# Optimization experiments

Hardware: AMD Instinct MI355X
Metric: run time of the kernel (lower is better)

The kernel has to match this reference:

```python
import jax, jax.numpy as jnp
import numpy as np

NUM_USERS = 100000
NUM_ITEMS = 50000
N = NUM_USERS + NUM_ITEMS
D = 64
NNZ = 4000000
BATCH = 8192
NUM_LAYERS = 3


def setup_inputs() -> dict:
    key = jax.random.key(0)
    k = jax.random.split(key, 8)
    return {
        "user_emb": jax.random.normal(k[0], (NUM_USERS, D), jnp.float32) * 0.1,
        "item_emb": jax.random.normal(k[1], (NUM_ITEMS, D), jnp.float32) * 0.1,
        # symmetric-normalized adjacency values (positive, ~1/degree scale)
        "adj_vals": jax.random.uniform(k[2], (NNZ,), jnp.float32) * (1.0 / 13.0),
        "adj_rows": jax.random.randint(k[3], (NNZ,), 0, N, jnp.int32),
        "adj_cols": jax.random.randint(k[4], (NNZ,), 0, N, jnp.int32),
        "user_idx": jax.random.randint(k[5], (BATCH,), 0, NUM_USERS, jnp.int32),
        "pos_idx": jax.random.randint(k[6], (BATCH,), 0, NUM_ITEMS, jnp.int32),
        "neg_idx": jax.random.randint(k[7], (BATCH,), 0, NUM_ITEMS, jnp.int32),
    }


def _propagate(user_emb, item_emb, adj_vals, adj_rows, adj_cols):
    # E0 = concat(user table, item table) along node axis -> [N, D]
    e = jnp.concatenate([user_emb, item_emb], axis=0)
    acc = e  # running sum over layer embeddings (E0 included)
    for _ in range(NUM_LAYERS):
        # SpMM: E <- A_norm @ E, via gather on cols + segment_sum on rows
        msg = adj_vals[:, None] * e[adj_cols]  # [NNZ, D]
        e = jax.ops.segment_sum(msg, adj_rows, num_segments=N)
        acc = acc + e
    final = acc / jnp.asarray(NUM_LAYERS + 1, e.dtype)  # mean-pool over layers
    return final


def reference(user_emb, item_emb, adj_vals, adj_rows, adj_cols,
              user_idx, pos_idx, neg_idx):
    final = _propagate(user_emb, item_emb, adj_vals, adj_rows, adj_cols)
    # split into user/item tables, then gather BPR triplets
    u = final[user_idx]                     # [B, D]
    p = final[NUM_USERS + pos_idx]          # [B, D]
    n = final[NUM_USERS + neg_idx]          # [B, D]
    pos_score = jnp.sum(u * p, axis=-1, keepdims=True)  # Dot(axes=1) -> [B,1]
    neg_score = jnp.sum(u * n, axis=-1, keepdims=True)
    return pos_score - neg_score
```

## Files before the change

kernel.cpp:

```cpp
#include <hip/hip_runtime.h>
#include <hip/hip_bf16.h>

#define D 64
#define MAXNB 1024
#define BIN_T 512
#define BIN_CHUNK 8192
#define BIN_EPT (BIN_CHUNK / BIN_T)
#define BUCKET_BITS 8
#define BUCKET_SIZE 256
#define COL_MASK 0x3FFFF
#define ROW_SHIFT 18

static __device__ __forceinline__ float bf_lo(unsigned v) {
  return __uint_as_float(v << 16);
}
static __device__ __forceinline__ float bf_hi(unsigned v) {
  return __uint_as_float(v & 0xffff0000u);
}
static __device__ __forceinline__ unsigned pack_bf2(float a, float b) {
  __hip_bfloat16 x = __float2bfloat16(a);
  __hip_bfloat16 y = __float2bfloat16(b);
  unsigned short ux = *reinterpret_cast<unsigned short*>(&x);
  unsigned short uy = *reinterpret_cast<unsigned short*>(&y);
  return (unsigned)ux | ((unsigned)uy << 16);
}

__global__ __launch_bounds__(256) void convert_kernel(
    const float4* __restrict__ ue, const float4* __restrict__ ie,
    uint2* __restrict__ out, int nu4, int total4,
    int* __restrict__ counts, int nbp1,
    const int* __restrict__ ui, const int* __restrict__ pi,
    const int* __restrict__ ni, int* __restrict__ list, int batch, int nu) {
  int i = blockIdx.x * blockDim.x + threadIdx.x;
  if (i < nbp1) counts[i] = 0;
  if (i < batch) {
    list[3 * i] = ui[i];
    list[3 * i + 1] = nu + pi[i];
    list[3 * i + 2] = nu + ni[i];
  }
  if (i >= total4) return;
  float4 v = (i < nu4) ? ue[i] : ie[i - nu4];
  out[i] = make_uint2(pack_bf2(v.x, v.y), pack_bf2(v.z, v.w));
}

__global__ __launch_bounds__(256) void bucket_hist_kernel(
    const int* __restrict__ rows, int* __restrict__ counts, int nnz, int nb) {
  __shared__ int h[MAXNB];
  int t = threadIdx.x;
  for (int i = t; i < nb; i += 256) h[i] = 0;
  __syncthreads();
  for (int e = blockIdx.x * 256 + t; e < nnz; e += gridDim.x * 256)
    atomicAdd(&h[rows[e] >> BUCKET_BITS], 1);
  __syncthreads();
  for (int i = t; i < nb; i += 256)
    if (h[i]) atomicAdd(&counts[i], h[i]);
}

__global__ __launch_bounds__(1024) void bucket_scan_kernel(
    const int* __restrict__ counts, int* __restrict__ base,
    int* __restrict__ cursor, int nb) {
  __shared__ int lds[1024];
  int t = threadIdx.x;
  int v = (t < nb) ? counts[t] : 0;
  lds[t] = v;
  __syncthreads();
  for (int off = 1; off < 1024; off <<= 1) {
    int add = (t >= off) ? lds[t - off] : 0;
    __syncthreads();
    lds[t] += add;
    __syncthreads();
  }
  if (t < nb) {
    base[t + 1] = lds[t];
    cursor[t + 1] = lds[t];
  }
  if (t == 0) {
    base[0] = 0;
    cursor[0] = 0;
  }
}

__global__ __launch_bounds__(BIN_T) void bin_kernel(
    const float* __restrict__ vals, const int* __restrict__ rows,
    const int* __restrict__ cols, int* __restrict__ cursor,
    int2* __restrict__ binned, int nnz, int nb) {
  __shared__ int lh[MAXNB];
  int t = threadIdx.x;
  long long base_e = (long long)blockIdx.x * BIN_CHUNK;
  int end_e = (int)((base_e + BIN_CHUNK < (long long)nnz) ? base_e + BIN_CHUNK
                                                          : (long long)nnz);
  for (int i = t; i < nb; i += BIN_T) lh[i] = 0;
  __syncthreads();
  int r[BIN_EPT];
  #pragma unroll
  for (int k = 0; k < BIN_EPT; ++k) {
    int e = (int)base_e + k * BIN_T + t;
    if (e < end_e) {
      r[k] = rows[e];
      atomicAdd(&lh[r[k] >> BUCKET_BITS], 1);
    } else {
      r[k] = -1;
    }
  }
  __syncthreads();
  for (int i = t; i < nb; i += BIN_T) {
    int c = lh[i];
    if (c) lh[i] = atomicAdd(&cursor[i], c);
  }
  __syncthreads();
  #pragma unroll
  for (int k = 0; k < BIN_EPT; ++k) {
    int e = (int)base_e + k * BIN_T + t;
    if (e < end_e) {
      int pos = atomicAdd(&lh[r[k] >> BUCKET_BITS], 1);
      binned[pos] = make_int2((cols[e] & COL_MASK) |
                                  ((r[k] & (BUCKET_SIZE - 1)) << ROW_SHIFT),
                              __float_as_int(vals[e]));
    }
  }
}

__global__ __launch_bounds__(512) void place_kernel(
    const int2* __restrict__ binned, const int* __restrict__ base,
    int2* __restrict__ edges, int* __restrict__ row_start, int nrows, int nb) {
  __shared__ int rh[BUCKET_SIZE];
  __shared__ int cur[BUCKET_SIZE];
  int b = blockIdx.x;
  int t = threadIdx.x;
  int start = base[b];
  int end = base[b + 1];
  int r0 = b << BUCKET_BITS;
  if (t < BUCKET_SIZE) rh[t] = 0;
  __syncthreads();
  for (int i = start + t; i < end; i += 512)
    atomicAdd(&rh[((unsigned)binned[i].x) >> ROW_SHIFT], 1);
  __syncthreads();
  int myc = (t < BUCKET_SIZE) ? rh[t] : 0;
  for (int off = 1; off < BUCKET_SIZE; off <<= 1) {
    int add = (t >= off && t < BUCKET_SIZE) ? rh[t - off] : 0;
    __syncthreads();
    if (t < BUCKET_SIZE) rh[t] += add;
    __syncthreads();
  }
  if (t < BUCKET_SIZE) {
    int excl = rh[t] - myc;
    int r = r0 + t;
    if (r < nrows) row_start[r] = start + excl;
    if (b == nb - 1 && t == 0) row_start[nrows] = end;
    cur[t] = start + excl;
  }
  __syncthreads();
  for (int i = start + t; i < end; i += 512) {
    int2 rec = binned[i];
    unsigned x = (unsigned)rec.x;
    int pos = atomicAdd(&cur[x >> ROW_SHIFT], 1);
    edges[pos] = make_int2((int)(x & COL_MASK), rec.y);
  }
}

__global__ __launch_bounds__(256) void spmm_bf16_kernel(
    const int* __restrict__ row_start, const int2* __restrict__ edges,
    const uint4* __restrict__ src,
    uint4* __restrict__ dst, int nrows) {
  int wid = (int)(((long long)blockIdx.x * blockDim.x + threadIdx.x) >> 6);
  if (wid >= nrows) return;
  int lane = threadIdx.x & 63;
  int sub = lane >> 3;
  int d8 = lane & 7;
  int s = row_start[wid];
  int e = row_start[wid + 1];
  float a0 = 0.f, a1 = 0.f, a2 = 0.f, a3 = 0.f;
  float a4 = 0.f, a5 = 0.f, a6 = 0.f, a7 = 0.f;
  int j = s;
  for (; j + 16 <= e; j += 16) {
    int2 E[2];
    uint4 V[2];
    #pragma unroll
    for (int k = 0; k < 2; ++k) E[k] = edges[j + 8 * k + sub];
    #pragma unroll
    for (int k = 0; k < 2; ++k)
      V[k] = src[((unsigned)E[k].x << 3) + (unsigned)d8];
    #pragma unroll
    for (int k = 0; k < 2; ++k) {
      float w = __int_as_float(E[k].y);
      a0 = fmaf(w, bf_lo(V[k].x), a0);
      a1 = fmaf(w, bf_hi(V[k].x), a1);
      a2 = fmaf(w, bf_lo(V[k].y), a2);
      a3 = fmaf(w, bf_hi(V[k].y), a3);
      a4 = fmaf(w, bf_lo(V[k].z), a4);
      a5 = fmaf(w, bf_hi(V[k].z), a5);
      a6 = fmaf(w, bf_lo(V[k].w), a6);
      a7 = fmaf(w, bf_hi(V[k].w), a7);
    }
  }
  for (; j < e; j += 8) {
    int idx = j + sub;
    bool ok = idx < e;
    int2 ed = edges[ok ? idx : (e - 1)];
    uint4 v = src[((unsigned)ed.x << 3) + (unsigned)d8];
    float w = ok ? __int_as_float(ed.y) : 0.f;
    a0 = fmaf(w, bf_lo(v.x), a0);
    a1 = fmaf(w, bf_hi(v.x), a1);
    a2 = fmaf(w, bf_lo(v.y), a2);
    a3 = fmaf(w, bf_hi(v.y), a3);
    a4 = fmaf(w, bf_lo(v.z), a4);
    a5 = fmaf(w, bf_hi(v.z), a5);
    a6 = fmaf(w, bf_lo(v.w), a6);
    a7 = fmaf(w, bf_hi(v.w), a7);
  }
  #pragma unroll
  for (int off = 32; off >= 8; off >>= 1) {
    a0 += __shfl_down(a0, off, 64);
    a1 += __shfl_down(a1, off, 64);
    a2 += __shfl_down(a2, off, 64);
    a3 += __shfl_down(a3, off, 64);
    a4 += __shfl_down(a4, off, 64);
    a5 += __shfl_down(a5, off, 64);
    a6 += __shfl_down(a6, off, 64);
    a7 += __shfl_down(a7, off, 64);
  }
  if (lane < 8)
    dst[((unsigned)wid << 3) + (unsigned)d8] =
        make_uint4(pack_bf2(a0, a1), pack_bf2(a2, a3),
                   pack_bf2(a4, a5), pack_bf2(a6, a7));
}

__global__ __launch_bounds__(256) void spmm_bf16_list_kernel(
    const int* __restrict__ row_start, const int2* __restrict__ edges,
    const uint4* __restrict__ src, uint4* __restrict__ dst,
    const int* __restrict__ list, int nlist) {
  int widx = (int)(((long long)blockIdx.x * blockDim.x + threadIdx.x) >> 6);
  if (widx >= nlist) return;
  int wid = list[widx];
  int lane = threadIdx.x & 63;
  int sub = lane >> 3;
  int d8 = lane & 7;
  int s = row_start[wid];
  int e = row_start[wid + 1];
  float a0 = 0.f, a1 = 0.f, a2 = 0.f, a3 = 0.f;
  float a4 = 0.f, a5 = 0.f, a6 = 0.f, a7 = 0.f;
  int j = s;
  for (; j + 16 <= e; j += 16) {
    int2 E[2];
    uint4 V[2];
    #pragma unroll
    for (int k = 0; k < 2; ++k) E[k] = edges[j + 8 * k + sub];
    #pragma unroll
    for (int k = 0; k < 2; ++k)
      V[k] = src[((unsigned)E[k].x << 3) + (unsigned)d8];
    #pragma unroll
    for (int k = 0; k < 2; ++k) {
      float w = __int_as_float(E[k].y);
      a0 = fmaf(w, bf_lo(V[k].x), a0);
      a1 = fmaf(w, bf_hi(V[k].x), a1);
      a2 = fmaf(w, bf_lo(V[k].y), a2);
      a3 = fmaf(w, bf_hi(V[k].y), a3);
      a4 = fmaf(w, bf_lo(V[k].z), a4);
      a5 = fmaf(w, bf_hi(V[k].z), a5);
      a6 = fmaf(w, bf_lo(V[k].w), a6);
      a7 = fmaf(w, bf_hi(V[k].w), a7);
    }
  }
  for (; j < e; j += 8) {
    int idx = j + sub;
    bool ok = idx < e;
    int2 ed = edges[ok ? idx : (e - 1)];
    uint4 v = src[((unsigned)ed.x << 3) + (unsigned)d8];
    float w = ok ? __int_as_float(ed.y) : 0.f;
    a0 = fmaf(w, bf_lo(v.x), a0);
    a1 = fmaf(w, bf_hi(v.x), a1);
    a2 = fmaf(w, bf_lo(v.y), a2);
    a3 = fmaf(w, bf_hi(v.y), a3);
    a4 = fmaf(w, bf_lo(v.z), a4);
    a5 = fmaf(w, bf_hi(v.z), a5);
    a6 = fmaf(w, bf_lo(v.w), a6);
    a7 = fmaf(w, bf_hi(v.w), a7);
  }
  #pragma unroll
  for (int off = 32; off >= 8; off >>= 1) {
    a0 += __shfl_down(a0, off, 64);
    a1 += __shfl_down(a1, off, 64);
    a2 += __shfl_down(a2, off, 64);
    a3 += __shfl_down(a3, off, 64);
    a4 += __shfl_down(a4, off, 64);
    a5 += __shfl_down(a5, off, 64);
    a6 += __shfl_down(a6, off, 64);
    a7 += __shfl_down(a7, off, 64);
  }
  if (lane < 8)
    dst[((unsigned)wid << 3) + (unsigned)d8] =
        make_uint4(pack_bf2(a0, a1), pack_bf2(a2, a3),
                   pack_bf2(a4, a5), pack_bf2(a6, a7));
}

__global__ __launch_bounds__(256) void score2_kernel(
    const float* __restrict__ ue, const float* __restrict__ ie,
    const unsigned* __restrict__ e1, const unsigned* __restrict__ e2,
    const unsigned* __restrict__ e3, const int* __restrict__ ui,
    const int* __restrict__ pi, const int* __restrict__ ni,
    float* __restrict__ out, int batch, int nu) {
  int w = (int)(((long long)blockIdx.x * blockDim.x + threadIdx.x) >> 6);
  int lane = threadIdx.x & 63;
  int half = lane >> 5;
  int d2 = lane & 31;
  int b = w * 2 + half;
  if (b >= batch) return;
  long long un = (long long)ui[b];
  int p = pi[b], n = ni[b];
  long long pn = (long long)(nu + p);
  long long nn_ = (long long)(nu + n);
  float2 U = *(const float2*)(ue + (un << 6) + (d2 << 1));
  float2 P = *(const float2*)(ie + ((long long)p << 6) + (d2 << 1));
  float2 Nv = *(const float2*)(ie + ((long long)n << 6) + (d2 << 1));
  unsigned v;
  v = e1[(un << 5) + d2]; U.x += bf_lo(v); U.y += bf_hi(v);
  v = e2[(un << 5) + d2]; U.x += bf_lo(v); U.y += bf_hi(v);
  v = e3[(un << 5) + d2]; U.x += bf_lo(v); U.y += bf_hi(v);
  v = e1[(pn << 5) + d2]; P.x += bf_lo(v); P.y += bf_hi(v);
  v = e2[(pn << 5) + d2]; P.x += bf_lo(v); P.y += bf_hi(v);
  v = e3[(pn << 5) + d2]; P.x += bf_lo(v); P.y += bf_hi(v);
  v = e1[(nn_ << 5) + d2]; Nv.x += bf_lo(v); Nv.y += bf_hi(v);
  v = e2[(nn_ << 5) + d2]; Nv.x += bf_lo(v); Nv.y += bf_hi(v);
  v = e3[(nn_ << 5) + d2]; Nv.x += bf_lo(v); Nv.y += bf_hi(v);
  float s = U.x * (P.x - Nv.x) + U.y * (P.y - Nv.y);
  #pragma unroll
  for (int off = 16; off; off >>= 1) s += __shfl_down(s, off, 32);
  if (d2 == 0) out[b] = s * (1.0f / 16.0f);
}

__global__ __launch_bounds__(256) void init_kernel(
    const float4* __restrict__ ue, const float4* __restrict__ ie,
    float4* __restrict__ e, float4* __restrict__ acc, int nu4, int total4) {
  int i = blockIdx.x * blockDim.x + threadIdx.x;
  if (i >= total4) return;
  float4 v = (i < nu4) ? ue[i] : ie[i - nu4];
  e[i] = v;
  acc[i] = v;
}

__global__ __launch_bounds__(256) void scatter_kernel(
    const float* __restrict__ vals, const int* __restrict__ rows,
    const int* __restrict__ cols, const float* __restrict__ src,
    float* __restrict__ dst, int nnz) {
  long long gid = (long long)blockIdx.x * blockDim.x + threadIdx.x;
  int e = (int)(gid >> 6);
  if (e >= nnz) return;
  int d = (int)(gid & 63);
  float w = vals[e];
  float x = src[((long long)cols[e] << 6) + d];
  atomicAdd(dst + (((long long)rows[e] << 6) + d), w * x);
}

__global__ __launch_bounds__(256) void acc_kernel(
    float4* __restrict__ acc, const float4* __restrict__ e, int total4) {
  int i = blockIdx.x * blockDim.x + threadIdx.x;
  if (i >= total4) return;
  float4 a = acc[i];
  float4 b = e[i];
  a.x += b.x; a.y += b.y; a.z += b.z; a.w += b.w;
  acc[i] = a;
}

__global__ __launch_bounds__(256) void score_kernel(
    const float* __restrict__ acc, const int* __restrict__ ui,
    const int* __restrict__ pi, const int* __restrict__ ni,
    float* __restrict__ out, int batch, int nu) {
  int wid = (int)(((long long)blockIdx.x * blockDim.x + threadIdx.x) >> 6);
  int lane = threadIdx.x & 63;
  if (wid >= batch) return;
  int u = ui[wid];
  int p = pi[wid];
  int n = ni[wid];
  float uv = acc[((long long)u << 6) + lane];
  float pv = acc[((long long)(nu + p) << 6) + lane];
  float nv = acc[((long long)(nu + n) << 6) + lane];
  float s = uv * (pv - nv);
  #pragma unroll
  for (int off = 32; off; off >>= 1) s += __shfl_down(s, off, 64);
  if (lane == 0) out[wid] = s * (1.0f / 16.0f);
}

static inline size_t align_up(size_t x) { return (x + 255) & ~(size_t)255; }

extern "C" void kernel_launch(void* const* d_in, const int* in_sizes, int n_in,
                              void* d_out, int out_size, void* d_ws, size_t ws_size,
                              hipStream_t stream) {
  const float* user_emb = (const float*)d_in[0];
  const float* item_emb = (const float*)d_in[1];
  const float* adj_vals = (const float*)d_in[2];
  const int* adj_rows = (const int*)d_in[3];
  const int* adj_cols = (const int*)d_in[4];
  const int* user_idx = (const int*)d_in[5];
  const int* pos_idx = (const int*)d_in[6];
  const int* neg_idx = (const int*)d_in[7];

  const int nnz = in_sizes[2];
  const int batch = in_sizes[5];
  const int nu = in_sizes[0] / D;
  const int ni = in_sizes[1] / D;
  const int nrows = nu + ni;
  const int nb = (nrows + BUCKET_SIZE - 1) / BUCKET_SIZE;
  const long long nd = (long long)nrows * D;
  const size_t nd_bytes = (size_t)nd * sizeof(float);
  const size_t bf_tbl = align_up((size_t)nrows * D * 2);
  const size_t edges_bytes = align_up((size_t)nnz * 8);

  const int total4 = (int)(nd / 4);
  const int nu4 = nu * D / 4;
  const int ew_blocks = (total4 + 255) / 256;

  const size_t need = 4 * bf_tbl + 2 * edges_bytes +
                      align_up((size_t)(nrows + 1) * 4) +
                      3 * align_up((size_t)(nb + 1) * 4) +
                      align_up((size_t)(3 * batch) * 4);
  const bool fast = (ws_size >= need) && (nb <= MAXNB) && (nrows <= COL_MASK);

  if (fast) {
    char* wp = (char*)d_ws;
    unsigned* e0b = (unsigned*)wp;    wp += bf_tbl;
    unsigned* e1 = (unsigned*)wp;     wp += bf_tbl;
    unsigned* e2 = (unsigned*)wp;     wp += bf_tbl;
    unsigned* e3 = (unsigned*)wp;     wp += bf_tbl;
    int2* edges = (int2*)wp;          wp += edges_bytes;
    int2* binned = (int2*)wp;         wp += edges_bytes;
    int* row_start = (int*)wp;        wp += align_up((size_t)(nrows + 1) * 4);
    int* base = (int*)wp;             wp += align_up((size_t)(nb + 1) * 4);
    int* counts = (int*)wp;           wp += align_up((size_t)(nb + 1) * 4);
    int* cursor = (int*)wp;           wp += align_up((size_t)(nb + 1) * 4);
    int* list = (int*)wp;

    convert_kernel<<<ew_blocks, 256, 0, stream>>>(
        (const float4*)user_emb, (const float4*)item_emb,
        (uint2*)e0b, nu4, total4, counts, nb + 1,
        user_idx, pos_idx, neg_idx, list, batch, nu);

    bucket_hist_kernel<<<1024, 256, 0, stream>>>(adj_rows, counts, nnz, nb);
    bucket_scan_kernel<<<1, 1024, 0, stream>>>(counts, base, cursor, nb);

    bin_kernel<<<(nnz + BIN_CHUNK - 1) / BIN_CHUNK, BIN_T, 0, stream>>>(
        adj_vals, adj_rows, adj_cols, cursor, binned, nnz, nb);
    place_kernel<<<nb, 512, 0, stream>>>(binned, base, edges, row_start,
                                         nrows, nb);

    const int spmm_blocks = (nrows + 3) / 4;
    spmm_bf16_kernel<<<spmm_blocks, 256, 0, stream>>>(
        row_start, edges, (const uint4*)e0b, (uint4*)e1, nrows);
    spmm_bf16_kernel<<<spmm_blocks, 256, 0, stream>>>(
        row_start, edges, (const uint4*)e1, (uint4*)e2, nrows);
    const int nlist = 3 * batch;
    spmm_bf16_list_kernel<<<(nlist + 3) / 4, 256, 0, stream>>>(
        row_start, edges, (const uint4*)e2, (uint4*)e3, list, nlist);

    score2_kernel<<<(batch / 2 + 3) / 4, 256, 0, stream>>>(
        user_emb, item_emb, e1, e2, e3, user_idx, pos_idx, neg_idx,
        (float*)d_out, batch, nu);
  } else {
    char* wp = (char*)d_ws;
    float* acc = (float*)wp;          wp += nd_bytes;
    float* e_a = (float*)wp;          wp += nd_bytes;
    float* e_b = (float*)wp;

    init_kernel<<<ew_blocks, 256, 0, stream>>>(
        (const float4*)user_emb, (const float4*)item_emb,
        (float4*)e_a, (float4*)acc, nu4, total4);
    const long long scatter_work = (long long)nnz * 64;
    const int scatter_blocks = (int)((scatter_work + 255) / 256);
    float* src = e_a;
    float* dst = e_b;
    for (int layer = 0; layer < 3; ++layer) {
      hipMemsetAsync(dst, 0, nd_bytes, stream);
      scatter_kernel<<<scatter_blocks, 256, 0, stream>>>(adj_vals, adj_rows,
                                                         adj_cols, src, dst, nnz);
      acc_kernel<<<ew_blocks, 256, 0, stream>>>((float4*)acc, (const float4*)dst,
                                                total4);
      float* t = src; src = dst; dst = t;
    }
    score_kernel<<<(batch + 3) / 4, 256, 0, stream>>>(
        acc, user_idx, pos_idx, neg_idx, (float*)d_out, batch, nu);
  }
}
```

Measured before the change: 291.9 us.

## Stage binned edges in LDS for coalesced bucket writes; widen buckets

The bin kernel now sorts each chunk's edges by bucket inside shared memory, using a block-wide prefix scan over bucket counts. It then writes them to global memory contiguously, finding each element's bucket by binary search, instead of scattering each edge straight to its global slot. Bucket size doubles to 512 rows, so there are about 293 buckets and one thread per bucket fits in the 512-thread block. Place_kernel is adjusted to work on 512-row buckets. The goal is coalesced global writes in the binning pass, at the cost of 64KB+ of LDS per block (lower occupancy), extra scan syncs and a binary search per element.

```diff
diff --git a/kernel.cpp b/kernel.cpp
--- a/kernel.cpp
+++ b/kernel.cpp
@@ -6,8 +6,8 @@
 #define BIN_T 512
 #define BIN_CHUNK 8192
 #define BIN_EPT (BIN_CHUNK / BIN_T)
-#define BUCKET_BITS 8
-#define BUCKET_SIZE 256
+#define BUCKET_BITS 9
+#define BUCKET_SIZE 512
 #define COL_MASK 0x3FFFF
 #define ROW_SHIFT 18
 
@@ -84,17 +84,21 @@
     const float* __restrict__ vals, const int* __restrict__ rows,
     const int* __restrict__ cols, int* __restrict__ cursor,
     int2* __restrict__ binned, int nnz, int nb) {
-  __shared__ int lh[MAXNB];
+  __shared__ int lh[BIN_T];
+  __shared__ int lstart[BIN_T];
+  __shared__ int gbase[BIN_T];
+  __shared__ int2 stage[BIN_CHUNK];
   int t = threadIdx.x;
-  long long base_e = (long long)blockIdx.x * BIN_CHUNK;
-  int end_e = (int)((base_e + BIN_CHUNK < (long long)nnz) ? base_e + BIN_CHUNK
-                                                          : (long long)nnz);
-  for (int i = t; i < nb; i += BIN_T) lh[i] = 0;
+  long long b0 = (long long)blockIdx.x * BIN_CHUNK;
+  int end_e = (int)((b0 + BIN_CHUNK < (long long)nnz) ? b0 + BIN_CHUNK
+                                                      : (long long)nnz);
+  int cnt = end_e - (int)b0;
+  lh[t] = 0;
   __syncthreads();
   int r[BIN_EPT];
   #pragma unroll
   for (int k = 0; k < BIN_EPT; ++k) {
-    int e = (int)base_e + k * BIN_T + t;
+    int e = (int)b0 + k * BIN_T + t;
     if (e < end_e) {
       r[k] = rows[e];
       atomicAdd(&lh[r[k] >> BUCKET_BITS], 1);
@@ -103,20 +107,42 @@
     }
   }
   __syncthreads();
-  for (int i = t; i < nb; i += BIN_T) {
-    int c = lh[i];
-    if (c) lh[i] = atomicAdd(&cursor[i], c);
+  int c = (t < nb) ? lh[t] : 0;
+  lstart[t] = c;
+  __syncthreads();
+  for (int off = 1; off < BIN_T; off <<= 1) {
+    int add = (t >= off) ? lstart[t - off] : 0;
+    __syncthreads();
+    lstart[t] += add;
+    __syncthreads();
+  }
+  int excl = lstart[t] - c;
+  int g = (t < nb && c) ? atomicAdd(&cursor[t], c) : 0;
+  __syncthreads();
+  if (t < nb) {
+    gbase[t] = g - excl;
+    lh[t] = excl;
+    lstart[t] = excl;
   }
   __syncthreads();
   #pragma unroll
   for (int k = 0; k < BIN_EPT; ++k) {
-    int e = (int)base_e + k * BIN_T + t;
+    int e = (int)b0 + k * BIN_T + t;
     if (e < end_e) {
       int pos = atomicAdd(&lh[r[k] >> BUCKET_BITS], 1);
-      binned[pos] = make_int2((cols[e] & COL_MASK) |
-                                  ((r[k] & (BUCKET_SIZE - 1)) << ROW_SHIFT),
-                              __float_as_int(vals[e]));
+      stage[pos] = make_int2((cols[e] & COL_MASK) |
+                                 ((r[k] & (BUCKET_SIZE - 1)) << ROW_SHIFT),
+                             __float_as_int(vals[e]));
     }
+  }
+  __syncthreads();
+  for (int i = t; i < cnt; i += BIN_T) {
+    int lo = 0, hi = nb - 1;
+    while (lo < hi) {
+      int mid = (lo + hi + 1) >> 1;
+      if (lstart[mid] <= i) lo = mid; else hi = mid - 1;
+    }
+    binned[gbase[lo] + i] = stage[i];
   }
 }
 
@@ -130,25 +156,23 @@
   int start = base[b];
   int end = base[b + 1];
   int r0 = b << BUCKET_BITS;
-  if (t < BUCKET_SIZE) rh[t] = 0;
+  rh[t] = 0;
   __syncthreads();
   for (int i = start + t; i < end; i += 512)
     atomicAdd(&rh[((unsigned)binned[i].x) >> ROW_SHIFT], 1);
   __syncthreads();
-  int myc = (t < BUCKET_SIZE) ? rh[t] : 0;
-  for (int off = 1; off < BUCKET_SIZE; off <<= 1) {
-    int add = (t >= off && t < BUCKET_SIZE) ? rh[t - off] : 0;
+  int myc = rh[t];
+  for (int off = 1; off < 512; off <<= 1) {
+    int add = (t >= off) ? rh[t - off] : 0;
     __syncthreads();
-    if (t < BUCKET_SIZE) rh[t] += add;
+    rh[t] += add;
     __syncthreads();
   }
-  if (t < BUCKET_SIZE) {
-    int excl = rh[t] - myc;
-    int r = r0 + t;
-    if (r < nrows) row_start[r] = start + excl;
-    if (b == nb - 1 && t == 0) row_start[nrows] = end;
-    cur[t] = start + excl;
-  }
+  int excl = rh[t] - myc;
+  int r = r0 + t;
+  if (r < nrows) row_start[r] = start + excl;
+  if (b == nb - 1 && t == 0) row_start[nrows] = end;
+  cur[t] = start + excl;
   __syncthreads();
   for (int i = start + t; i < end; i += 512) {
     int2 rec = binned[i];
@@ -413,7 +437,7 @@
                       align_up((size_t)(nrows + 1) * 4) +
                       3 * align_up((size_t)(nb + 1) * 4) +
                       align_up((size_t)(3 * batch) * 4);
-  const bool fast = (ws_size >= need) && (nb <= MAXNB) && (nrows <= COL_MASK);
+  const bool fast = (ws_size >= need) && (nb <= BIN_T) && (nrows <= COL_MASK);
 
   if (fast) {
     char* wp = (char*)d_ws;
```

Measured after the change: 288.4 us. Within noise of the previous version (-1.2%).
